# Optimization experiments

Measured on AMD Instinct MI355X. Metric: run time of the kernel, lower is better.

## Reference

```python
import jax, jax.numpy as jnp
import numpy as np

B, S, H = 1, 2048, 2048
NH, NKV, HD = 16, 4, 128
F, E, TOPK = 4096, 8, 2
EPS = 1e-5
THETA = 10000.0
NEG = -1e30


def setup_inputs() -> dict:
    key = jax.random.key(0)
    ks = jax.random.split(key, 12)
    s = 0.02
    f32 = jnp.float32
    return {
        "positions": jnp.arange(S, dtype=jnp.int32),
        "hidden_states": jax.random.normal(ks[0], (B, S, H), f32),
        "wq": jax.random.normal(ks[1], (H, NH * HD), f32) * s,
        "wk": jax.random.normal(ks[2], (H, NKV * HD), f32) * s,
        "wv": jax.random.normal(ks[3], (H, NKV * HD), f32) * s,
        "wo": jax.random.normal(ks[4], (NH * HD, H), f32) * s,
        "w_gate": jax.random.normal(ks[5], (H, E), f32) * s,
        "w1": jax.random.normal(ks[6], (E, H, F), f32) * s,
        "w2": jax.random.normal(ks[7], (E, F, H), f32) * s,
        "w3": jax.random.normal(ks[8], (E, H, F), f32) * s,
        "ln_in": jnp.ones((H,), f32),
        "ln_post": jnp.ones((H,), f32),
    }


def rmsnorm(x, w):
    var = jnp.mean(jnp.square(x.astype(jnp.float32)), axis=-1, keepdims=True)
    return (x.astype(jnp.float32) * jax.lax.rsqrt(var + EPS)).astype(x.dtype) * w


def apply_rope(x, positions):
    # x: [B, S, n, HD], neox style (rotate halves)
    half = HD // 2
    inv_freq = 1.0 / (THETA ** (jnp.arange(half, dtype=jnp.float32) * 2.0 / HD))
    ang = positions.astype(jnp.float32)[:, None] * inv_freq  # [S, half]
    cos = jnp.cos(ang)[None, :, None, :]
    sin = jnp.sin(ang)[None, :, None, :]
    x1, x2 = jnp.split(x, 2, axis=-1)
    return jnp.concatenate([x1 * cos - x2 * sin, x2 * cos + x1 * sin], axis=-1).astype(x.dtype)


def decoder_layer(positions, x, wq, wk, wv, wo, w_gate, w1, w2, w3, ln_in, ln_post):
    # residual is None branch: residual = x; h = input_layernorm(x)
    residual = x
    h = rmsnorm(x, ln_in)
    # --- attention ---
    q = (h @ wq).reshape(B, S, NH, HD)
    k = (h @ wk).reshape(B, S, NKV, HD)
    v = (h @ wv).reshape(B, S, NKV, HD)
    q = apply_rope(q, positions)
    k = apply_rope(k, positions)
    rep = NH // NKV  # GQA: repeat kv heads
    k = jnp.repeat(k, rep, axis=2)
    v = jnp.repeat(v, rep, axis=2)
    scores = jnp.einsum("bqhd,bkhd->bhqk", q, k) * (HD ** -0.5)
    causal = jnp.tril(jnp.ones((S, S), bool))
    scores = jnp.where(causal[None, None], scores, NEG)
    attn = jax.nn.softmax(scores, axis=-1)
    o = jnp.einsum("bhqk,bkhd->bqhd", attn, v).reshape(B, S, NH * HD) @ wo
    # --- fused add + post-attention RMSNorm ---
    residual = o + residual
    h = rmsnorm(residual, ln_post)
    # --- MoE: dense all-expert compute, mask-weighted combine ---
    xt = h.reshape(-1, H)  # [T, H]
    logits = xt @ w_gate
    rw = jax.nn.softmax(logits.astype(jnp.float32), axis=-1)  # [T, E]
    w_top, idx = jax.lax.top_k(rw, TOPK)
    w_top = w_top / jnp.sum(w_top, axis=-1, keepdims=True)
    T = xt.shape[0]
    combine = jnp.zeros((T, E), jnp.float32).at[jnp.arange(T)[:, None], idx].add(w_top)
    a = jnp.einsum("th,ehf->etf", xt, w1)  # [E, T, F]
    g = jax.nn.silu(a) * jnp.einsum("th,ehf->etf", xt, w3)
    out = jnp.einsum("etf,efh->eth", g, w2)  # [E, T, H]
    moe = jnp.einsum("eth,te->th", out, combine.astype(xt.dtype))
    return moe.reshape(B, S, H), residual


def reference(positions, hidden_states, wq, wk, wv, wo, w_gate, w1, w2, w3, ln_in, ln_post):
    return decoder_layer(positions, hidden_states, wq, wk, wv, wo, w_gate, w1, w2, w3, ln_in, ln_post)
```

## Files before the change

kernel.cpp:

```cpp
#include <hip/hip_runtime.h>

typedef _Float16 f16x8 __attribute__((ext_vector_type(8)));
typedef float f32x4 __attribute__((ext_vector_type(4)));

#define DEV __device__ __forceinline__

struct alignas(16) H8 { _Float16 h[8]; };
struct alignas(8)  H4 { _Float16 h[4]; };

DEV f32x4 mfma16(f16x8 a, f16x8 b, f32x4 c) {
  return __builtin_amdgcn_mfma_f32_16x16x32_f16(a, b, c, 0, 0, 0);
}

DEV f16x8 frag_b36(const _Float16* b, int n, int kc) {
  const unsigned long long* p = (const unsigned long long*)(b + n*36 + kc*8);
  union { unsigned long long u[2]; f16x8 v; } r;
  r.u[0] = p[0]; r.u[1] = p[1];
  return r.v;
}

DEV float block_sum(float v, volatile float* red, int tid) {
  #pragma unroll
  for (int mm = 1; mm < 64; mm <<= 1) v += __shfl_xor(v, mm);
  if ((tid & 63) == 0) red[tid >> 6] = v;
  __syncthreads();
  return red[0] + red[1] + red[2] + red[3];
}

__global__ __launch_bounds__(256) void k_rmsnorm_split(
    const float* __restrict__ x, const float* __restrict__ w,
    _Float16* __restrict__ hi, _Float16* __restrict__ lo) {
  __shared__ float red[4];
  int row = blockIdx.x, tid = threadIdx.x;
  const float* xr = x + (size_t)row*2048 + tid*8;
  float xs[8];
  *(float4*)&xs[0] = *(const float4*)xr;
  *(float4*)&xs[4] = *(const float4*)(xr + 4);
  float ss = 0.f;
  #pragma unroll
  for (int j = 0; j < 8; ++j) ss += xs[j]*xs[j];
  float tot = block_sum(ss, red, tid);
  float sc = 1.0f / sqrtf(tot*(1.0f/2048.0f) + 1e-5f);
  const float* wr = w + tid*8;
  H8 ph, pl;
  #pragma unroll
  for (int j = 0; j < 8; ++j) {
    float o = xs[j]*sc*wr[j];
    _Float16 hh = (_Float16)o;
    ph.h[j] = hh; pl.h[j] = (_Float16)(o - (float)hh);
  }
  *(H8*)(hi + (size_t)row*2048 + tid*8) = ph;
  *(H8*)(lo + (size_t)row*2048 + tid*8) = pl;
}

template<int AMODE, bool RESID>
__global__ __launch_bounds__(256) void k_gemm(
    const void* __restrict__ Ahi, const void* __restrict__ Alo,
    const float* __restrict__ B, int N, int K,
    float* __restrict__ C,
    const float* __restrict__ resid_in, float* __restrict__ resid_out) {
  const int tid = threadIdx.x;
  const int l = tid & 63, w = tid >> 6;
  const int wm = w >> 1, wn = w & 1;
  const int row0 = blockIdx.y * 128, col0 = blockIdx.x * 128;

  __shared__ _Float16 aHi[128*32], aLo[128*32];
  __shared__ _Float16 bHi[128*36], bLo[128*36];

  f32x4 acc[4][4] = {};

  const int rS = tid >> 1, khalf = tid & 1;
  const int bn = tid & 127, bkg = tid >> 7;

  for (int k0 = 0; k0 < K; k0 += 32) {
    __syncthreads();
    {
      int c0 = khalf*2;
      int d0 = rS*32 + ((c0    ) ^ (rS&3))*8;
      int d1 = rS*32 + ((c0 + 1) ^ (rS&3))*8;
      if constexpr (AMODE == 0) {
        const _Float16* ah = (const _Float16*)Ahi + (size_t)(row0 + rS)*K + k0 + khalf*16;
        const _Float16* al = (const _Float16*)Alo + (size_t)(row0 + rS)*K + k0 + khalf*16;
        *(H8*)&aHi[d0] = *(const H8*)ah;
        *(H8*)&aHi[d1] = *(const H8*)(ah + 8);
        *(H8*)&aLo[d0] = *(const H8*)al;
        *(H8*)&aLo[d1] = *(const H8*)(al + 8);
      } else {
        const float* af = (const float*)Ahi + (size_t)(row0 + rS)*K + k0 + khalf*16;
        H8 ph0, pl0, ph1, pl1;
        #pragma unroll
        for (int j = 0; j < 8; ++j) {
          float x0 = af[j], x1 = af[8 + j];
          _Float16 h0 = (_Float16)x0, h1 = (_Float16)x1;
          ph0.h[j] = h0; pl0.h[j] = (_Float16)(x0 - (float)h0);
          ph1.h[j] = h1; pl1.h[j] = (_Float16)(x1 - (float)h1);
        }
        *(H8*)&aHi[d0] = ph0; *(H8*)&aHi[d1] = ph1;
        *(H8*)&aLo[d0] = pl0; *(H8*)&aLo[d1] = pl1;
      }
    }
    {
      const float* bp = B + (size_t)(k0 + bkg*16)*N + col0 + bn;
      float tv[16];
      #pragma unroll
      for (int i = 0; i < 16; ++i) tv[i] = bp[(size_t)i*N];
      #pragma unroll
      for (int q_ = 0; q_ < 4; ++q_) {
        H4 ph, pl;
        #pragma unroll
        for (int j = 0; j < 4; ++j) {
          float x = tv[q_*4 + j];
          _Float16 hh = (_Float16)x;
          ph.h[j] = hh; pl.h[j] = (_Float16)(x - (float)hh);
        }
        int ei = bn*36 + bkg*16 + q_*4;
        *(H4*)&bHi[ei] = ph;
        *(H4*)&bLo[ei] = pl;
      }
    }
    __syncthreads();
    {
      const int kc = l >> 4;
      f16x8 ah[4], al4[4];
      #pragma unroll
      for (int m = 0; m < 4; ++m) {
        int mr = wm*64 + m*16 + (l & 15);
        int cc = (kc ^ (mr & 3))*8;
        ah[m]  = *(const f16x8*)&aHi[mr*32 + cc];
        al4[m] = *(const f16x8*)&aLo[mr*32 + cc];
      }
      #pragma unroll
      for (int n = 0; n < 4; ++n) {
        int nr = wn*64 + n*16 + (l & 15);
        f16x8 bh = frag_b36(bHi, nr, kc);
        f16x8 bl = frag_b36(bLo, nr, kc);
        #pragma unroll
        for (int m = 0; m < 4; ++m) {
          acc[m][n] = mfma16(ah[m],  bh, acc[m][n]);
          acc[m][n] = mfma16(ah[m],  bl, acc[m][n]);
          acc[m][n] = mfma16(al4[m], bh, acc[m][n]);
        }
      }
    }
  }
  #pragma unroll
  for (int m = 0; m < 4; ++m)
    #pragma unroll
    for (int n = 0; n < 4; ++n)
      #pragma unroll
      for (int r = 0; r < 4; ++r) {
        int row = row0 + wm*64 + m*16 + (l>>4)*4 + r;
        int col = col0 + wn*64 + n*16 + (l&15);
        float v = acc[m][n][r];
        if constexpr (RESID) {
          size_t idx = (size_t)row*2048 + col;
          v += resid_in[idx];
          resid_out[idx] = v;
        } else {
          C[(size_t)row*N + col] = v;
        }
      }
}

__global__ __launch_bounds__(256) void k_rope(
    float* __restrict__ buf, const int* __restrict__ pos, int nh) {
  int s = blockIdx.x;
  int hh = blockIdx.y*4 + (threadIdx.x >> 6);
  int d = threadIdx.x & 63;
  float p = (float)pos[s];
  double ex = ((double)(2*d)/128.0) * 9.210340371976184;
  float pw = (float)exp(ex);
  float inv = 1.0f / pw;
  float ang = p * inv;
  float cs = cosf(ang), sn = sinf(ang);
  float* b = buf + (size_t)s*(nh*128) + hh*128 + d;
  float x1 = b[0], x2 = b[64];
  b[0]  = x1*cs - x2*sn;
  b[64] = x2*cs + x1*sn;
}

__global__ __launch_bounds__(256) void k_attn(
    const float* __restrict__ q, const float* __restrict__ k,
    const float* __restrict__ v, float* __restrict__ o) {
  const int qt = blockIdx.x, h = blockIdx.y;
  const int tid = threadIdx.x, l = tid & 63, w = tid >> 6;
  const int qb = qt*64, qw = qb + w*16;
  const int kvh = h >> 2;

  __shared__ _Float16 kHi[32*128], kLo[32*128];
  __shared__ _Float16 vHi[128*32], vLo[128*32];
  __shared__ _Float16 pHi[4][16*40], pLo[4][16*40];

  f16x8 qh[4], ql[4];
  {
    int qrow = qw + (l & 15);
    const float* qp = q + (size_t)qrow*2048 + h*128 + (l>>4)*8;
    #pragma unroll
    for (int c = 0; c < 4; ++c)
      #pragma unroll
      for (int j = 0; j < 8; ++j) {
        float x = qp[c*32 + j];
        _Float16 hh = (_Float16)x;
        qh[c][j] = hh; ql[c][j] = (_Float16)(x - (float)hh);
      }
  }

  float mrun[4], lrun[4];
  f32x4 oacc[8] = {};
  #pragma unroll
  for (int r = 0; r < 4; ++r) { mrun[r] = -1e30f; lrun[r] = 0.f; }

  const int srow = tid >> 3, sc = (tid & 7)*2;

  for (int kv0 = 0; kv0 <= qb + 32; kv0 += 32) {
    __syncthreads();
    {
      const float* kp = k + (size_t)(kv0 + srow)*512 + kvh*128 + sc*8;
      const float* vp = v + (size_t)(kv0 + srow)*512 + kvh*128 + sc*8;
      #pragma unroll
      for (int cc = 0; cc < 2; ++cc) {
        int c = sc + cc;
        H8 ph, pl;
        #pragma unroll
        for (int j = 0; j < 8; ++j) {
          float x = kp[cc*8 + j];
          _Float16 hh = (_Float16)x;
          ph.h[j] = hh; pl.h[j] = (_Float16)(x - (float)hh);
        }
        int di = srow*128 + (c ^ (srow & 7))*8;
        *(H8*)&kHi[di] = ph;
        *(H8*)&kLo[di] = pl;
        #pragma unroll
        for (int j = 0; j < 8; ++j) {
          float x = vp[cc*8 + j];
          _Float16 hh = (_Float16)x;
          _Float16 ll = (_Float16)(x - (float)hh);
          int d = c*8 + j;
          int vi = d*32 + (((srow>>3) ^ (d&3)))*8 + (srow & 7);
          vHi[vi] = hh; vLo[vi] = ll;
        }
      }
    }
    __syncthreads();
    if (kv0 <= qw + 15) {
      f32x4 s[2] = {};
      #pragma unroll
      for (int nt = 0; nt < 2; ++nt) {
        int krow = nt*16 + (l & 15);
        #pragma unroll
        for (int c = 0; c < 4; ++c) {
          int ch = (c*4 + (l>>4)) ^ (krow & 7);
          f16x8 bh = *(const f16x8*)&kHi[krow*128 + ch*8];
          f16x8 bl = *(const f16x8*)&kLo[krow*128 + ch*8];
          s[nt] = mfma16(qh[c], bh, s[nt]);
          s[nt] = mfma16(qh[c], bl, s[nt]);
          s[nt] = mfma16(ql[c], bh, s[nt]);
        }
      }
      const float SC = 0.08838834764831845f;
      float sv[2][4];
      #pragma unroll
      for (int nt = 0; nt < 2; ++nt)
        #pragma unroll
        for (int r = 0; r < 4; ++r) {
          float val = s[nt][r]*SC;
          int qg = qw + (l>>4)*4 + r;
          int kg = kv0 + nt*16 + (l & 15);
          sv[nt][r] = (kg > qg) ? -1e30f : val;
        }
      float tm[4];
      #pragma unroll
      for (int r = 0; r < 4; ++r) tm[r] = fmaxf(sv[0][r], sv[1][r]);
      #pragma unroll
      for (int mm = 1; mm < 16; mm <<= 1)
        #pragma unroll
        for (int r = 0; r < 4; ++r) tm[r] = fmaxf(tm[r], __shfl_xor(tm[r], mm));
      float alpha[4], rs[4];
      #pragma unroll
      for (int r = 0; r < 4; ++r) {
        float mn = fmaxf(mrun[r], tm[r]);
        alpha[r] = expf(mrun[r] - mn);
        mrun[r] = mn;
      }
      float pv[2][4];
      #pragma unroll
      for (int nt = 0; nt < 2; ++nt)
        #pragma unroll
        for (int r = 0; r < 4; ++r) pv[nt][r] = expf(sv[nt][r] - mrun[r]);
      #pragma unroll
      for (int r = 0; r < 4; ++r) rs[r] = pv[0][r] + pv[1][r];
      #pragma unroll
      for (int mm = 1; mm < 16; mm <<= 1)
        #pragma unroll
        for (int r = 0; r < 4; ++r) rs[r] += __shfl_xor(rs[r], mm);
      #pragma unroll
      for (int r = 0; r < 4; ++r) lrun[r] = lrun[r]*alpha[r] + rs[r];
      #pragma unroll
      for (int dt = 0; dt < 8; ++dt)
        #pragma unroll
        for (int r = 0; r < 4; ++r) oacc[dt][r] *= alpha[r];
      #pragma unroll
      for (int nt = 0; nt < 2; ++nt)
        #pragma unroll
        for (int r = 0; r < 4; ++r) {
          float x = pv[nt][r];
          _Float16 hh = (_Float16)x;
          int qr = (l>>4)*4 + r, kc = nt*16 + (l & 15);
          pHi[w][qr*40 + kc] = hh;
          pLo[w][qr*40 + kc] = (_Float16)(x - (float)hh);
        }
      f16x8 pa = *(const f16x8*)&pHi[w][(l&15)*40 + (l>>4)*8];
      f16x8 pb = *(const f16x8*)&pLo[w][(l&15)*40 + (l>>4)*8];
      #pragma unroll
      for (int dt = 0; dt < 8; ++dt) {
        int d = dt*16 + (l & 15);
        int ch = ((l>>4) ^ (d & 3))*8;
        f16x8 vh = *(const f16x8*)&vHi[d*32 + ch];
        f16x8 vl = *(const f16x8*)&vLo[d*32 + ch];
        oacc[dt] = mfma16(pa, vh, oacc[dt]);
        oacc[dt] = mfma16(pa, vl, oacc[dt]);
        oacc[dt] = mfma16(pb, vh, oacc[dt]);
      }
    }
  }
  #pragma unroll
  for (int dt = 0; dt < 8; ++dt)
    #pragma unroll
    for (int r = 0; r < 4; ++r) {
      int qg = qw + (l>>4)*4 + r;
      o[(size_t)qg*2048 + h*128 + dt*16 + (l&15)] = oacc[dt][r] / lrun[r];
    }
}

__global__ __launch_bounds__(256) void k_postnorm_gate(
    const float* __restrict__ resid, const float* __restrict__ wln,
    const float* __restrict__ wg, _Float16* __restrict__ h2,
    float* __restrict__ logits) {
  __shared__ float red[4];
  __shared__ float red2[4][8];
  int row = blockIdx.x, tid = threadIdx.x;
  const float* xr = resid + (size_t)row*2048 + tid*8;
  float xs[8];
  *(float4*)&xs[0] = *(const float4*)xr;
  *(float4*)&xs[4] = *(const float4*)(xr + 4);
  float ss = 0.f;
  #pragma unroll
  for (int j = 0; j < 8; ++j) ss += xs[j]*xs[j];
  float tot = block_sum(ss, red, tid);
  float sc = 1.0f/sqrtf(tot*(1.0f/2048.0f) + 1e-5f);
  const float* wr = wln + tid*8;
  float hv[8];
  H8 ph;
  #pragma unroll
  for (int j = 0; j < 8; ++j) {
    hv[j] = xs[j]*sc*wr[j];
    ph.h[j] = (_Float16)hv[j];
  }
  *(H8*)(h2 + (size_t)row*2048 + tid*8) = ph;
  float lg[8] = {0,0,0,0,0,0,0,0};
  const float* wgp = wg + (size_t)tid*8*8;
  #pragma unroll
  for (int j = 0; j < 8; ++j)
    #pragma unroll
    for (int e = 0; e < 8; ++e) lg[e] += hv[j]*wgp[j*8 + e];
  #pragma unroll
  for (int mm = 1; mm < 64; mm <<= 1)
    #pragma unroll
    for (int e = 0; e < 8; ++e) lg[e] += __shfl_xor(lg[e], mm);
  if ((tid & 63) == 0)
    #pragma unroll
    for (int e = 0; e < 8; ++e) red2[tid>>6][e] = lg[e];
  __syncthreads();
  if (tid < 8)
    logits[(size_t)row*8 + tid] = red2[0][tid]+red2[1][tid]+red2[2][tid]+red2[3][tid];
}

__global__ __launch_bounds__(256) void k_route(
    const float* __restrict__ logits, int* __restrict__ counts,
    int* __restrict__ slot_tok, float* __restrict__ slot_w) {
  int t = blockIdx.x*256 + threadIdx.x;
  if (t >= 2048) return;
  float lg[8];
  #pragma unroll
  for (int e = 0; e < 8; ++e) lg[e] = logits[t*8 + e];
  int a = 0; float la = lg[0];
  #pragma unroll
  for (int e = 1; e < 8; ++e) if (lg[e] > la) { la = lg[e]; a = e; }
  int b = -1; float lb = -3e38f;
  #pragma unroll
  for (int e = 0; e < 8; ++e) if (e != a && lg[e] > lb) { lb = lg[e]; b = e; }
  float wa = 1.f/(1.f + expf(lb - la));
  float wb = 1.f - wa;
  int sa = atomicAdd(&counts[a], 1);
  slot_tok[a*2048 + sa] = t; slot_w[a*2048 + sa] = wa;
  int sb = atomicAdd(&counts[b], 1);
  slot_tok[b*2048 + sb] = t; slot_w[b*2048 + sb] = wb;
}

__global__ void k_scan(const int* __restrict__ counts, int* __restrict__ offs) {
  if (threadIdx.x == 0) {
    int o_ = 0;
    #pragma unroll
    for (int e = 0; e < 8; ++e) { offs[e] = o_; o_ += counts[e]; }
  }
}

__global__ __launch_bounds__(256) void k_moe1(
    const _Float16* __restrict__ h2, const float* __restrict__ w1,
    const float* __restrict__ w3, const int* __restrict__ counts,
    const int* __restrict__ offs, const int* __restrict__ slot_tok,
    _Float16* __restrict__ g) {
  int bid = blockIdx.x;
  int e = bid >> 10, mt = (bid >> 6) & 15, nt = bid & 63;
  int cnt = counts[e];
  if (mt*128 >= cnt) return;
  const int tid = threadIdx.x, l = tid & 63, w = tid >> 6;
  const int wm = w >> 1, wn = w & 1;
  __shared__ _Float16 aT[128*32];
  __shared__ _Float16 b1[64*36], b3[64*36];
  const int rS = tid >> 1, khalf = tid & 1;
  int slot = mt*128 + rS;
  int tok = (slot < cnt) ? slot_tok[e*2048 + slot] : 0;
  const _Float16* arow = h2 + (size_t)tok*2048;
  const float* w1e = w1 + (size_t)e*2048*4096;
  const float* w3e = w3 + (size_t)e*2048*4096;
  const int bn = tid & 63, bkg = tid >> 6;
  f32x4 acc1[4][2] = {}, acc3[4][2] = {};
  for (int k0 = 0; k0 < 2048; k0 += 32) {
    __syncthreads();
    {
      const _Float16* ap = arow + k0 + khalf*16;
      int c0 = khalf*2;
      *(H8*)&aT[rS*32 + ((c0  )^(rS&3))*8] = *(const H8*)ap;
      *(H8*)&aT[rS*32 + ((c0+1)^(rS&3))*8] = *(const H8*)(ap + 8);
    }
    {
      const float* bp1 = w1e + (size_t)(k0 + bkg*8)*4096 + nt*64 + bn;
      const float* bp3 = w3e + (size_t)(k0 + bkg*8)*4096 + nt*64 + bn;
      float t1[8], t3[8];
      #pragma unroll
      for (int i = 0; i < 8; ++i) { t1[i] = bp1[(size_t)i*4096]; t3[i] = bp3[(size_t)i*4096]; }
      #pragma unroll
      for (int q_ = 0; q_ < 2; ++q_) {
        H4 p1, p3;
        #pragma unroll
        for (int j = 0; j < 4; ++j) { p1.h[j] = (_Float16)t1[q_*4+j]; p3.h[j] = (_Float16)t3[q_*4+j]; }
        int ei = bn*36 + bkg*8 + q_*4;
        *(H4*)&b1[ei] = p1;
        *(H4*)&b3[ei] = p3;
      }
    }
    __syncthreads();
    {
      const int kc = l >> 4;
      f16x8 a_[4];
      #pragma unroll
      for (int m = 0; m < 4; ++m) {
        int mr = wm*64 + m*16 + (l & 15);
        a_[m] = *(const f16x8*)&aT[mr*32 + (kc ^ (mr&3))*8];
      }
      #pragma unroll
      for (int n = 0; n < 2; ++n) {
        int nr = wn*32 + n*16 + (l & 15);
        f16x8 bb1 = frag_b36(b1, nr, kc);
        f16x8 bb3 = frag_b36(b3, nr, kc);
        #pragma unroll
        for (int m = 0; m < 4; ++m) {
          acc1[m][n] = mfma16(a_[m], bb1, acc1[m][n]);
          acc3[m][n] = mfma16(a_[m], bb3, acc3[m][n]);
        }
      }
    }
  }
  int ge = offs[e];
  #pragma unroll
  for (int m = 0; m < 4; ++m)
    #pragma unroll
    for (int n = 0; n < 2; ++n)
      #pragma unroll
      for (int r = 0; r < 4; ++r) {
        int srow2 = mt*128 + wm*64 + m*16 + (l>>4)*4 + r;
        if (srow2 < cnt) {
          float x1 = acc1[m][n][r], x3 = acc3[m][n][r];
          float gg = (x1/(1.f + expf(-x1)))*x3;
          int col = nt*64 + wn*32 + n*16 + (l&15);
          g[(size_t)(ge + srow2)*4096 + col] = (_Float16)gg;
        }
      }
}

__global__ __launch_bounds__(256) void k_moe2(
    const _Float16* __restrict__ g, const float* __restrict__ w2,
    const int* __restrict__ counts, const int* __restrict__ offs,
    const int* __restrict__ slot_tok, const float* __restrict__ slot_w,
    float* __restrict__ out) {
  int bid = blockIdx.x;
  int e = bid >> 8, mt = (bid >> 4) & 15, nt = bid & 15;
  int cnt = counts[e];
  if (mt*128 >= cnt) return;
  const int tid = threadIdx.x, l = tid & 63, w = tid >> 6;
  const int wm = w >> 1, wn = w & 1;
  __shared__ _Float16 aT[128*32];
  __shared__ _Float16 bT[128*36];
  const int rS = tid >> 1, khalf = tid & 1;
  int ge = offs[e];
  int slot = mt*128 + rS;
  const _Float16* arow = g + (size_t)(ge + (slot < cnt ? slot : 0))*4096;
  const float* w2e = w2 + (size_t)e*4096*2048;
  const int bn = tid & 127, bkg = tid >> 7;
  f32x4 acc[4][4] = {};
  for (int k0 = 0; k0 < 4096; k0 += 32) {
    __syncthreads();
    {
      const _Float16* ap = arow + k0 + khalf*16;
      int c0 = khalf*2;
      *(H8*)&aT[rS*32 + ((c0  )^(rS&3))*8] = *(const H8*)ap;
      *(H8*)&aT[rS*32 + ((c0+1)^(rS&3))*8] = *(const H8*)(ap + 8);
    }
    {
      const float* bp = w2e + (size_t)(k0 + bkg*16)*2048 + nt*128 + bn;
      float tv[16];
      #pragma unroll
      for (int i = 0; i < 16; ++i) tv[i] = bp[(size_t)i*2048];
      #pragma unroll
      for (int q_ = 0; q_ < 4; ++q_) {
        H4 ph;
        #pragma unroll
        for (int j = 0; j < 4; ++j) ph.h[j] = (_Float16)tv[q_*4+j];
        *(H4*)&bT[bn*36 + bkg*16 + q_*4] = ph;
      }
    }
    __syncthreads();
    {
      const int kc = l >> 4;
      f16x8 a_[4];
      #pragma unroll
      for (int m = 0; m < 4; ++m) {
        int mr = wm*64 + m*16 + (l&15);
        a_[m] = *(const f16x8*)&aT[mr*32 + (kc ^ (mr&3))*8];
      }
      #pragma unroll
      for (int n = 0; n < 4; ++n) {
        f16x8 bb = frag_b36(bT, wn*64 + n*16 + (l&15), kc);
        #pragma unroll
        for (int m = 0; m < 4; ++m) acc[m][n] = mfma16(a_[m], bb, acc[m][n]);
      }
    }
  }
  #pragma unroll
  for (int m = 0; m < 4; ++m)
    #pragma unroll
    for (int r = 0; r < 4; ++r) {
      int srow2 = mt*128 + wm*64 + m*16 + (l>>4)*4 + r;
      if (srow2 < cnt) {
        int tok = slot_tok[e*2048 + srow2];
        float wt = slot_w[e*2048 + srow2];
        #pragma unroll
        for (int n = 0; n < 4; ++n) {
          int col = nt*128 + wn*64 + n*16 + (l&15);
          atomicAdd(&out[(size_t)tok*2048 + col], wt*acc[m][n][r]);
        }
      }
    }
}

extern "C" void kernel_launch(void* const* d_in, const int* in_sizes, int n_in,
                              void* d_out, int out_size, void* d_ws, size_t ws_size,
                              hipStream_t stream) {
  const int*   positions = (const int*)d_in[0];
  const float* x   = (const float*)d_in[1];
  const float* wq  = (const float*)d_in[2];
  const float* wk  = (const float*)d_in[3];
  const float* wv  = (const float*)d_in[4];
  const float* wo  = (const float*)d_in[5];
  const float* wg  = (const float*)d_in[6];
  const float* w1  = (const float*)d_in[7];
  const float* w2  = (const float*)d_in[8];
  const float* w3  = (const float*)d_in[9];
  const float* ln_in   = (const float*)d_in[10];
  const float* ln_post = (const float*)d_in[11];

  float* moe_out   = (float*)d_out;
  float* resid_out = (float*)d_out + (size_t)4194304;

  char* ws = (char*)d_ws;
  _Float16* h_hi   = (_Float16*)(ws);
  _Float16* h_lo   = (_Float16*)(ws + 8388608);
  float*    qbuf   = (float*)(ws + 16777216);
  float*    kbuf   = (float*)(ws + 33554432);
  float*    vbuf   = (float*)(ws + 37748736);
  float*    attn   = (float*)(ws + 41943040);
  _Float16* h2     = (_Float16*)(ws + 58720256);
  float*    logits = (float*)(ws + 67108864);
  int*      counts = (int*)(ws + 67174400);
  int*      offs   = (int*)(ws + 67174656);
  int*      slot_tok = (int*)(ws + 67174912);
  float*    slot_w   = (float*)(ws + 67240448);
  _Float16* gbuf   = (_Float16*)ws;

  hipMemsetAsync(moe_out, 0, (size_t)4194304*4, stream);
  hipMemsetAsync(counts, 0, 32, stream);

  k_rmsnorm_split<<<2048, 256, 0, stream>>>(x, ln_in, h_hi, h_lo);
  k_gemm<0,false><<<dim3(16,16), 256, 0, stream>>>(h_hi, h_lo, wq, 2048, 2048, qbuf, nullptr, nullptr);
  k_gemm<0,false><<<dim3(4,16),  256, 0, stream>>>(h_hi, h_lo, wk,  512, 2048, kbuf, nullptr, nullptr);
  k_gemm<0,false><<<dim3(4,16),  256, 0, stream>>>(h_hi, h_lo, wv,  512, 2048, vbuf, nullptr, nullptr);
  k_rope<<<dim3(2048,4), 256, 0, stream>>>(qbuf, positions, 16);
  k_rope<<<dim3(2048,1), 256, 0, stream>>>(kbuf, positions, 4);
  k_attn<<<dim3(32,16), 256, 0, stream>>>(qbuf, kbuf, vbuf, attn);
  k_gemm<1,true><<<dim3(16,16), 256, 0, stream>>>(attn, nullptr, wo, 2048, 2048, nullptr, x, resid_out);
  k_postnorm_gate<<<2048, 256, 0, stream>>>(resid_out, ln_post, wg, h2, logits);
  k_route<<<8, 256, 0, stream>>>(logits, counts, slot_tok, slot_w);
  k_scan<<<1, 64, 0, stream>>>(counts, offs);
  k_moe1<<<8192, 256, 0, stream>>>(h2, w1, w3, counts, offs, slot_tok, gbuf);
  k_moe2<<<2048, 256, 0, stream>>>(gbuf, w2, counts, offs, slot_tok, slot_w, moe_out);
}
```

Measured before the change: 1.293 ms.

## Double-buffer MoE GEMMs with 256-row tiles and emit split-fp16 attention output

The two MoE expert GEMMs move to 512-thread blocks with 256-row M tiles and double-buffered shared memory. Each iteration prefetches the next K-slice into registers while the current one computes, so only one barrier is needed per step and each fp32 weight tile is reused across twice as many token rows. The attention kernel now writes its output already split into fp16 hi/lo, so the output projection GEMM loads fp16 directly instead of converting fp32 in its inner loop. The cost is higher LDS use per block and more padded work when an expert's token count is not a multiple of 256.

```diff
diff --git a/kernel.cpp b/kernel.cpp
--- a/kernel.cpp
+++ b/kernel.cpp
@@ -53,9 +53,9 @@
   *(H8*)(lo + (size_t)row*2048 + tid*8) = pl;
 }
 
-template<int AMODE, bool RESID>
+template<bool RESID>
 __global__ __launch_bounds__(256) void k_gemm(
-    const void* __restrict__ Ahi, const void* __restrict__ Alo,
+    const _Float16* __restrict__ Ahi, const _Float16* __restrict__ Alo,
     const float* __restrict__ B, int N, int K,
     float* __restrict__ C,
     const float* __restrict__ resid_in, float* __restrict__ resid_out) {
@@ -78,26 +78,12 @@
       int c0 = khalf*2;
       int d0 = rS*32 + ((c0    ) ^ (rS&3))*8;
       int d1 = rS*32 + ((c0 + 1) ^ (rS&3))*8;
-      if constexpr (AMODE == 0) {
-        const _Float16* ah = (const _Float16*)Ahi + (size_t)(row0 + rS)*K + k0 + khalf*16;
-        const _Float16* al = (const _Float16*)Alo + (size_t)(row0 + rS)*K + k0 + khalf*16;
-        *(H8*)&aHi[d0] = *(const H8*)ah;
-        *(H8*)&aHi[d1] = *(const H8*)(ah + 8);
-        *(H8*)&aLo[d0] = *(const H8*)al;
-        *(H8*)&aLo[d1] = *(const H8*)(al + 8);
-      } else {
-        const float* af = (const float*)Ahi + (size_t)(row0 + rS)*K + k0 + khalf*16;
-        H8 ph0, pl0, ph1, pl1;
-        #pragma unroll
-        for (int j = 0; j < 8; ++j) {
-          float x0 = af[j], x1 = af[8 + j];
-          _Float16 h0 = (_Float16)x0, h1 = (_Float16)x1;
-          ph0.h[j] = h0; pl0.h[j] = (_Float16)(x0 - (float)h0);
-          ph1.h[j] = h1; pl1.h[j] = (_Float16)(x1 - (float)h1);
-        }
-        *(H8*)&aHi[d0] = ph0; *(H8*)&aHi[d1] = ph1;
-        *(H8*)&aLo[d0] = pl0; *(H8*)&aLo[d1] = pl1;
-      }
+      const _Float16* ah = Ahi + (size_t)(row0 + rS)*K + k0 + khalf*16;
+      const _Float16* al = Alo + (size_t)(row0 + rS)*K + k0 + khalf*16;
+      *(H8*)&aHi[d0] = *(const H8*)ah;
+      *(H8*)&aHi[d1] = *(const H8*)(ah + 8);
+      *(H8*)&aLo[d0] = *(const H8*)al;
+      *(H8*)&aLo[d1] = *(const H8*)(al + 8);
     }
     {
       const float* bp = B + (size_t)(k0 + bkg*16)*N + col0 + bn;
@@ -181,7 +167,8 @@
 
 __global__ __launch_bounds__(256) void k_attn(
     const float* __restrict__ q, const float* __restrict__ k,
-    const float* __restrict__ v, float* __restrict__ o) {
+    const float* __restrict__ v,
+    _Float16* __restrict__ o_hi, _Float16* __restrict__ o_lo) {
   const int qt = blockIdx.x, h = blockIdx.y;
   const int tid = threadIdx.x, l = tid & 63, w = tid >> 6;
   const int qb = qt*64, qw = qb + w*16;
@@ -328,7 +315,11 @@
     #pragma unroll
     for (int r = 0; r < 4; ++r) {
       int qg = qw + (l>>4)*4 + r;
-      o[(size_t)qg*2048 + h*128 + dt*16 + (l&15)] = oacc[dt][r] / lrun[r];
+      float ov = oacc[dt][r] / lrun[r];
+      _Float16 hh = (_Float16)ov;
+      size_t idx = (size_t)qg*2048 + h*128 + dt*16 + (l&15);
+      o_hi[idx] = hh;
+      o_lo[idx] = (_Float16)(ov - (float)hh);
     }
 }
 
@@ -405,73 +396,81 @@
   }
 }
 
-__global__ __launch_bounds__(256) void k_moe1(
+__global__ __launch_bounds__(512, 4) void k_moe1(
     const _Float16* __restrict__ h2, const float* __restrict__ w1,
     const float* __restrict__ w3, const int* __restrict__ counts,
     const int* __restrict__ offs, const int* __restrict__ slot_tok,
     _Float16* __restrict__ g) {
   int bid = blockIdx.x;
-  int e = bid >> 10, mt = (bid >> 6) & 15, nt = bid & 63;
+  int e = bid >> 9, mt = (bid >> 6) & 7, nt = bid & 63;
   int cnt = counts[e];
-  if (mt*128 >= cnt) return;
+  if (mt*256 >= cnt) return;
   const int tid = threadIdx.x, l = tid & 63, w = tid >> 6;
   const int wm = w >> 1, wn = w & 1;
-  __shared__ _Float16 aT[128*32];
-  __shared__ _Float16 b1[64*36], b3[64*36];
+  __shared__ _Float16 aT[2][256*32];
+  __shared__ _Float16 bS[2][2][64*36];
   const int rS = tid >> 1, khalf = tid & 1;
-  int slot = mt*128 + rS;
-  int tok = (slot < cnt) ? slot_tok[e*2048 + slot] : 0;
+  int slot = mt*256 + rS;
+  int tok = slot_tok[e*2048 + (slot < cnt ? slot : 0)];
   const _Float16* arow = h2 + (size_t)tok*2048;
-  const float* w1e = w1 + (size_t)e*2048*4096;
-  const float* w3e = w3 + (size_t)e*2048*4096;
+  const float* w1e = w1 + (size_t)e*2048*4096 + nt*64 + (tid & 63);
+  const float* w3e = w3 + (size_t)e*2048*4096 + nt*64 + (tid & 63);
   const int bn = tid & 63, bkg = tid >> 6;
   f32x4 acc1[4][2] = {}, acc3[4][2] = {};
-  for (int k0 = 0; k0 < 2048; k0 += 32) {
+  H8 ta0, ta1; float tb1[4], tb3[4];
+
+  auto LOAD = [&](int k0) {
+    const _Float16* ap = arow + k0 + khalf*16;
+    ta0 = *(const H8*)ap;
+    ta1 = *(const H8*)(ap + 8);
+    const float* p1 = w1e + (size_t)(k0 + bkg*4)*4096;
+    const float* p3 = w3e + (size_t)(k0 + bkg*4)*4096;
+    #pragma unroll
+    for (int i = 0; i < 4; ++i) { tb1[i] = p1[(size_t)i*4096]; tb3[i] = p3[(size_t)i*4096]; }
+  };
+  auto WRITE = [&](int buf) {
+    int c0 = khalf*2;
+    *(H8*)&aT[buf][rS*32 + ((c0  )^(rS&3))*8] = ta0;
+    *(H8*)&aT[buf][rS*32 + ((c0+1)^(rS&3))*8] = ta1;
+    H4 h1, h3;
+    #pragma unroll
+    for (int j = 0; j < 4; ++j) { h1.h[j] = (_Float16)tb1[j]; h3.h[j] = (_Float16)tb3[j]; }
+    *(H4*)&bS[buf][0][bn*36 + bkg*4] = h1;
+    *(H4*)&bS[buf][1][bn*36 + bkg*4] = h3;
+  };
+  auto COMPUTE = [&](int buf) {
+    const int kc = l >> 4;
+    f16x8 a_[4];
+    #pragma unroll
+    for (int m = 0; m < 4; ++m) {
+      int mr = wm*64 + m*16 + (l & 15);
+      a_[m] = *(const f16x8*)&aT[buf][mr*32 + (kc ^ (mr&3))*8];
+    }
+    #pragma unroll
+    for (int n = 0; n < 2; ++n) {
+      int nr = wn*32 + n*16 + (l & 15);
+      f16x8 bb1 = frag_b36(&bS[buf][0][0], nr, kc);
+      f16x8 bb3 = frag_b36(&bS[buf][1][0], nr, kc);
+      #pragma unroll
+      for (int m = 0; m < 4; ++m) {
+        acc1[m][n] = mfma16(a_[m], bb1, acc1[m][n]);
+        acc3[m][n] = mfma16(a_[m], bb3, acc3[m][n]);
+      }
+    }
+  };
+
+  LOAD(0); WRITE(0); LOAD(32);
+  __syncthreads();
+  #pragma unroll 2
+  for (int kk = 0; kk < 64; ++kk) {
+    COMPUTE(kk & 1);
+    if (kk < 63) {
+      WRITE((kk+1) & 1);
+      if (kk < 62) LOAD((kk+2)*32);
+    }
     __syncthreads();
-    {
-      const _Float16* ap = arow + k0 + khalf*16;
-      int c0 = khalf*2;
-      *(H8*)&aT[rS*32 + ((c0  )^(rS&3))*8] = *(const H8*)ap;
-      *(H8*)&aT[rS*32 + ((c0+1)^(rS&3))*8] = *(const H8*)(ap + 8);
-    }
-    {
-      const float* bp1 = w1e + (size_t)(k0 + bkg*8)*4096 + nt*64 + bn;
-      const float* bp3 = w3e + (size_t)(k0 + bkg*8)*4096 + nt*64 + bn;
-      float t1[8], t3[8];
-      #pragma unroll
-      for (int i = 0; i < 8; ++i) { t1[i] = bp1[(size_t)i*4096]; t3[i] = bp3[(size_t)i*4096]; }
-      #pragma unroll
-      for (int q_ = 0; q_ < 2; ++q_) {
-        H4 p1, p3;
-        #pragma unroll
-        for (int j = 0; j < 4; ++j) { p1.h[j] = (_Float16)t1[q_*4+j]; p3.h[j] = (_Float16)t3[q_*4+j]; }
-        int ei = bn*36 + bkg*8 + q_*4;
-        *(H4*)&b1[ei] = p1;
-        *(H4*)&b3[ei] = p3;
-      }
-    }
-    __syncthreads();
-    {
-      const int kc = l >> 4;
-      f16x8 a_[4];
-      #pragma unroll
-      for (int m = 0; m < 4; ++m) {
-        int mr = wm*64 + m*16 + (l & 15);
-        a_[m] = *(const f16x8*)&aT[mr*32 + (kc ^ (mr&3))*8];
-      }
-      #pragma unroll
-      for (int n = 0; n < 2; ++n) {
-        int nr = wn*32 + n*16 + (l & 15);
-        f16x8 bb1 = frag_b36(b1, nr, kc);
-        f16x8 bb3 = frag_b36(b3, nr, kc);
-        #pragma unroll
-        for (int m = 0; m < 4; ++m) {
-          acc1[m][n] = mfma16(a_[m], bb1, acc1[m][n]);
-          acc3[m][n] = mfma16(a_[m], bb3, acc3[m][n]);
-        }
-      }
-    }
-  }
+  }
+
   int ge = offs[e];
   #pragma unroll
   for (int m = 0; m < 4; ++m)
@@ -479,7 +478,7 @@
     for (int n = 0; n < 2; ++n)
       #pragma unroll
       for (int r = 0; r < 4; ++r) {
-        int srow2 = mt*128 + wm*64 + m*16 + (l>>4)*4 + r;
+        int srow2 = mt*256 + wm*64 + m*16 + (l>>4)*4 + r;
         if (srow2 < cnt) {
           float x1 = acc1[m][n][r], x3 = acc3[m][n][r];
           float gg = (x1/(1.f + expf(-x1)))*x3;
@@ -489,69 +488,81 @@
       }
 }
 
-__global__ __launch_bounds__(256) void k_moe2(
+__global__ __launch_bounds__(512, 4) void k_moe2(
     const _Float16* __restrict__ g, const float* __restrict__ w2,
     const int* __restrict__ counts, const int* __restrict__ offs,
     const int* __restrict__ slot_tok, const float* __restrict__ slot_w,
     float* __restrict__ out) {
   int bid = blockIdx.x;
-  int e = bid >> 8, mt = (bid >> 4) & 15, nt = bid & 15;
+  int e = bid >> 7, mt = (bid >> 4) & 7, nt = bid & 15;
   int cnt = counts[e];
-  if (mt*128 >= cnt) return;
+  if (mt*256 >= cnt) return;
   const int tid = threadIdx.x, l = tid & 63, w = tid >> 6;
   const int wm = w >> 1, wn = w & 1;
-  __shared__ _Float16 aT[128*32];
-  __shared__ _Float16 bT[128*36];
+  __shared__ _Float16 aT[2][256*32];
+  __shared__ _Float16 bT[2][128*36];
   const int rS = tid >> 1, khalf = tid & 1;
   int ge = offs[e];
-  int slot = mt*128 + rS;
+  int slot = mt*256 + rS;
   const _Float16* arow = g + (size_t)(ge + (slot < cnt ? slot : 0))*4096;
-  const float* w2e = w2 + (size_t)e*4096*2048;
+  const float* w2e = w2 + (size_t)e*4096*2048 + nt*128 + (tid & 127);
   const int bn = tid & 127, bkg = tid >> 7;
   f32x4 acc[4][4] = {};
-  for (int k0 = 0; k0 < 4096; k0 += 32) {
+  H8 ta0, ta1; float tb[8];
+
+  auto LOAD = [&](int k0) {
+    const _Float16* ap = arow + k0 + khalf*16;
+    ta0 = *(const H8*)ap;
+    ta1 = *(const H8*)(ap + 8);
+    const float* p = w2e + (size_t)(k0 + bkg*8)*2048;
+    #pragma unroll
+    for (int i = 0; i < 8; ++i) tb[i] = p[(size_t)i*2048];
+  };
+  auto WRITE = [&](int buf) {
+    int c0 = khalf*2;
+    *(H8*)&aT[buf][rS*32 + ((c0  )^(rS&3))*8] = ta0;
+    *(H8*)&aT[buf][rS*32 + ((c0+1)^(rS&3))*8] = ta1;
+    #pragma unroll
+    for (int q_ = 0; q_ < 2; ++q_) {
+      H4 ph;
+      #pragma unroll
+      for (int j = 0; j < 4; ++j) ph.h[j] = (_Float16)tb[q_*4 + j];
+      *(H4*)&bT[buf][bn*36 + bkg*8 + q_*4] = ph;
+    }
+  };
+  auto COMPUTE = [&](int buf) {
+    const int kc = l >> 4;
+    f16x8 a_[4];
+    #pragma unroll
+    for (int m = 0; m < 4; ++m) {
+      int mr = wm*64 + m*16 + (l & 15);
+      a_[m] = *(const f16x8*)&aT[buf][mr*32 + (kc ^ (mr&3))*8];
+    }
+    #pragma unroll
+    for (int n = 0; n < 4; ++n) {
+      f16x8 bb = frag_b36(&bT[buf][0], wn*64 + n*16 + (l&15), kc);
+      #pragma unroll
+      for (int m = 0; m < 4; ++m) acc[m][n] = mfma16(a_[m], bb, acc[m][n]);
+    }
+  };
+
+  LOAD(0); WRITE(0); LOAD(32);
+  __syncthreads();
+  #pragma unroll 2
+  for (int kk = 0; kk < 128; ++kk) {
+    COMPUTE(kk & 1);
+    if (kk < 127) {
+      WRITE((kk+1) & 1);
+      if (kk < 126) LOAD((kk+2)*32);
+    }
     __syncthreads();
-    {
-      const _Float16* ap = arow + k0 + khalf*16;
-      int c0 = khalf*2;
-      *(H8*)&aT[rS*32 + ((c0  )^(rS&3))*8] = *(const H8*)ap;
-      *(H8*)&aT[rS*32 + ((c0+1)^(rS&3))*8] = *(const H8*)(ap + 8);
-    }
-    {
-      const float* bp = w2e + (size_t)(k0 + bkg*16)*2048 + nt*128 + bn;
-      float tv[16];
-      #pragma unroll
-      for (int i = 0; i < 16; ++i) tv[i] = bp[(size_t)i*2048];
-      #pragma unroll
-      for (int q_ = 0; q_ < 4; ++q_) {
-        H4 ph;
-        #pragma unroll
-        for (int j = 0; j < 4; ++j) ph.h[j] = (_Float16)tv[q_*4+j];
-        *(H4*)&bT[bn*36 + bkg*16 + q_*4] = ph;
-      }
-    }
-    __syncthreads();
-    {
-      const int kc = l >> 4;
-      f16x8 a_[4];
-      #pragma unroll
-      for (int m = 0; m < 4; ++m) {
-        int mr = wm*64 + m*16 + (l&15);
-        a_[m] = *(const f16x8*)&aT[mr*32 + (kc ^ (mr&3))*8];
-      }
-      #pragma unroll
-      for (int n = 0; n < 4; ++n) {
-        f16x8 bb = frag_b36(bT, wn*64 + n*16 + (l&15), kc);
-        #pragma unroll
-        for (int m = 0; m < 4; ++m) acc[m][n] = mfma16(a_[m], bb, acc[m][n]);
-      }
-    }
-  }
+  }
+
   #pragma unroll
   for (int m = 0; m < 4; ++m)
     #pragma unroll
     for (int r = 0; r < 4; ++r) {
-      int srow2 = mt*128 + wm*64 + m*16 + (l>>4)*4 + r;
+      int srow2 = mt*256 + wm*64 + m*16 + (l>>4)*4 + r;
       if (srow2 < cnt) {
         int tok = slot_tok[e*2048 + srow2];
         float wt = slot_w[e*2048 + srow2];
@@ -589,7 +600,8 @@
   float*    qbuf   = (float*)(ws + 16777216);
   float*    kbuf   = (float*)(ws + 33554432);
   float*    vbuf   = (float*)(ws + 37748736);
-  float*    attn   = (float*)(ws + 41943040);
+  _Float16* o_hi   = (_Float16*)(ws + 41943040);
+  _Float16* o_lo   = (_Float16*)(ws + 50331648);
   _Float16* h2     = (_Float16*)(ws + 58720256);
   float*    logits = (float*)(ws + 67108864);
   int*      counts = (int*)(ws + 67174400);
@@ -602,16 +614,16 @@
   hipMemsetAsync(counts, 0, 32, stream);
 
   k_rmsnorm_split<<<2048, 256, 0, stream>>>(x, ln_in, h_hi, h_lo);
-  k_gemm<0,false><<<dim3(16,16), 256, 0, stream>>>(h_hi, h_lo, wq, 2048, 2048, qbuf, nullptr, nullptr);
-  k_gemm<0,false><<<dim3(4,16),  256, 0, stream>>>(h_hi, h_lo, wk,  512, 2048, kbuf, nullptr, nullptr);
-  k_gemm<0,false><<<dim3(4,16),  256, 0, stream>>>(h_hi, h_lo, wv,  512, 2048, vbuf, nullptr, nullptr);
+  k_gemm<false><<<dim3(16,16), 256, 0, stream>>>(h_hi, h_lo, wq, 2048, 2048, qbuf, nullptr, nullptr);
+  k_gemm<false><<<dim3(4,16),  256, 0, stream>>>(h_hi, h_lo, wk,  512, 2048, kbuf, nullptr, nullptr);
+  k_gemm<false><<<dim3(4,16),  256, 0, stream>>>(h_hi, h_lo, wv,  512, 2048, vbuf, nullptr, nullptr);
   k_rope<<<dim3(2048,4), 256, 0, stream>>>(qbuf, positions, 16);
   k_rope<<<dim3(2048,1), 256, 0, stream>>>(kbuf, positions, 4);
-  k_attn<<<dim3(32,16), 256, 0, stream>>>(qbuf, kbuf, vbuf, attn);
-  k_gemm<1,true><<<dim3(16,16), 256, 0, stream>>>(attn, nullptr, wo, 2048, 2048, nullptr, x, resid_out);
+  k_attn<<<dim3(32,16), 256, 0, stream>>>(qbuf, kbuf, vbuf, o_hi, o_lo);
+  k_gemm<true><<<dim3(16,16), 256, 0, stream>>>(o_hi, o_lo, wo, 2048, 2048, nullptr, x, resid_out);
   k_postnorm_gate<<<2048, 256, 0, stream>>>(resid_out, ln_post, wg, h2, logits);
   k_route<<<8, 256, 0, stream>>>(logits, counts, slot_tok, slot_w);
   k_scan<<<1, 64, 0, stream>>>(counts, offs);
-  k_moe1<<<8192, 256, 0, stream>>>(h2, w1, w3, counts, offs, slot_tok, gbuf);
-  k_moe2<<<2048, 256, 0, stream>>>(gbuf, w2, counts, offs, slot_tok, slot_w, moe_out);
-}
+  k_moe1<<<4096, 512, 0, stream>>>(h2, w1, w3, counts, offs, slot_tok, gbuf);
+  k_moe2<<<1024, 512, 0, stream>>>(gbuf, w2, counts, offs, slot_tok, slot_w, moe_out);
+}
```

After: 1.753 ms. +35.6%, slower.
